# Performance work log

Hardware: AMD Instinct MI355X
Metric: run time of the kernel (lower is better)

Reference implementation:

```python
import jax, jax.numpy as jnp
import numpy as np

N = 20000      # total nodes across the mini-batch of graphs
E = 320000     # edges (avg degree 16)
B = 16         # graphs in the batch
HEADS = 8
EPS_BN = 1e-5
NEG_SLOPE = 0.2


def _lin(k, fan_in, fan_out):
    return (jax.random.normal(k, (fan_in, fan_out), jnp.float32) / np.float32(np.sqrt(fan_in)))


def setup_inputs() -> dict:
    key = jax.random.key(0)
    ks = jax.random.split(key, 24)
    inp = {}
    inp["x"] = jax.random.normal(ks[0], (N, 3), jnp.float32)
    inp["edge_index"] = jax.random.randint(ks[1], (2, E), 0, N, dtype=jnp.int32)
    inp["batch"] = jnp.sort(jax.random.randint(ks[2], (N,), 0, B, dtype=jnp.int32))
    # GATConv params: lin weight [in, heads*out], att_src/att_dst [heads,out], bias [heads*out]
    dims = [(3, 16), (128, 32), (256, 64)]
    for i, (cin, cout) in enumerate(dims, start=1):
        base = 3 + 5 * i
        inp[f"W{i}"] = _lin(ks[base], cin, HEADS * cout)
        inp[f"as{i}"] = jax.random.normal(ks[base + 1], (HEADS, cout), jnp.float32) * 0.1
        inp[f"ad{i}"] = jax.random.normal(ks[base + 2], (HEADS, cout), jnp.float32) * 0.1
        inp[f"b{i}"] = jnp.zeros((HEADS * cout,), jnp.float32)
        inp[f"g{i}"] = jnp.ones((HEADS * cout,), jnp.float32)
        inp[f"be{i}"] = jnp.zeros((HEADS * cout,), jnp.float32)
    inp["fcW"] = _lin(ks[20], 512, 10)
    inp["fcb"] = jnp.zeros((10,), jnp.float32)
    return inp


def gat_layer(x, src, dst, W, a_s, a_d, bias, heads, out_ch):
    n = x.shape[0]
    h = (x @ W).reshape(n, heads, out_ch)              # [N,H,C]
    al_s = jnp.einsum('nhc,hc->nh', h, a_s)            # [N,H]
    al_d = jnp.einsum('nhc,hc->nh', h, a_d)
    e = jax.nn.leaky_relu(al_s[src] + al_d[dst], NEG_SLOPE)   # [E,H]
    m = jax.ops.segment_max(e, dst, num_segments=n)    # per-dst softmax (stable)
    e = jnp.exp(e - m[dst])
    denom = jax.ops.segment_sum(e, dst, num_segments=n)
    alpha = e / (denom[dst] + 1e-16)
    out = jax.ops.segment_sum(h[src] * alpha[:, :, None], dst, num_segments=n)
    return out.reshape(n, heads * out_ch) + bias


def bn_relu(x, g, b):
    mu = x.mean(0)
    var = x.var(0)  # biased, as torch BN uses for normalization
    return jax.nn.relu((x - mu) * jax.lax.rsqrt(var + EPS_BN) * g + b)


def reference(x, edge_index, batch, W1, as1, ad1, b1, g1, be1,
              W2, as2, ad2, b2, g2, be2, W3, as3, ad3, b3, g3, be3, fcW, fcb):
    n = x.shape[0]
    loops = jnp.arange(n, dtype=edge_index.dtype)
    src = jnp.concatenate([edge_index[0], loops])  # add_self_loops=True (PyG default)
    dst = jnp.concatenate([edge_index[1], loops])
    h = bn_relu(gat_layer(x, src, dst, W1, as1, ad1, b1, HEADS, 16), g1, be1)
    h = bn_relu(gat_layer(h, src, dst, W2, as2, ad2, b2, HEADS, 32), g2, be2)
    h = bn_relu(gat_layer(h, src, dst, W3, as3, ad3, b3, HEADS, 64), g3, be3)
    pooled = jax.ops.segment_max(h, batch, num_segments=B)  # global_max_pool
    return pooled @ fcW + fcb
```

## Files before the change

kernel.cpp:

```cpp
#include <hip/hip_runtime.h>
#include <hip/hip_bf16.h>

#define HEADS 8
#define EPS_BN 1e-5f
#define NEG_SLOPE 0.2f
#define BN_NB 256

typedef __attribute__((ext_vector_type(8))) short bf16x8;
typedef __attribute__((ext_vector_type(4))) float f32x4;

__device__ __forceinline__ float bf2f(unsigned short u) {
    return __uint_as_float(((unsigned int)u) << 16);
}

__device__ __forceinline__ unsigned short f2bf(float f) {
    __hip_bfloat16 b = __float2bfloat16(f);
    return *reinterpret_cast<unsigned short*>(&b);
}

__device__ __forceinline__ void gld_lds16(const ushort* g, ushort* l) {
    __builtin_amdgcn_global_load_lds(
        (const __attribute__((address_space(1))) unsigned int*)g,
        (__attribute__((address_space(3))) unsigned int*)l, 16, 0, 0);
}


__global__ void count_kernel(const int* __restrict__ ei, int E, int N, int* __restrict__ counts) {
    int i = blockIdx.x * blockDim.x + threadIdx.x;
    int total = E + N;
    if (i >= total) return;
    int d = (i < E) ? ei[E + i] : (i - E);
    atomicAdd(&counts[d], 1);
}

__global__ __launch_bounds__(1024) void scan_kernel(const int* __restrict__ counts,
                                                    int* __restrict__ offs, int n) {
    __shared__ int tile[1024];
    int tid = threadIdx.x;
    int carry = 0;
    for (int base = 0; base < n; base += 1024) {
        int v = (base + tid < n) ? counts[base + tid] : 0;
        tile[tid] = v;
        __syncthreads();
        for (int off = 1; off < 1024; off <<= 1) {
            int t = (tid >= off) ? tile[tid - off] : 0;
            __syncthreads();
            tile[tid] += t;
            __syncthreads();
        }
        if (base + tid < n) offs[base + tid + 1] = carry + tile[tid];
        carry += tile[1023];
        __syncthreads();
    }
    if (tid == 0) offs[0] = 0;
}

__global__ void scatter_kernel(const int* __restrict__ ei, int E, int N,
                               const int* __restrict__ offs, int* __restrict__ cursor,
                               int* __restrict__ csr_src) {
    int i = blockIdx.x * blockDim.x + threadIdx.x;
    int total = E + N;
    if (i >= total) return;
    int s, d;
    if (i < E) { s = ei[i]; d = ei[E + i]; } else { s = i - E; d = i - E; }
    int slot = atomicAdd(&cursor[d], 1);
    csr_src[offs[d] + slot] = s;
}


__global__ __launch_bounds__(256) void linear1_al_tr_kernel(const float* __restrict__ x,
                                                            const float* __restrict__ W,
                                                            const float* __restrict__ a_s,
                                                            const float* __restrict__ a_d,
                                                            ushort* __restrict__ h,
                                                            float* __restrict__ als,
                                                            float* __restrict__ ald, int N,
                                                            const float* __restrict__ W2,
                                                            ushort* __restrict__ Wt2,
                                                            const float* __restrict__ W3,
                                                            ushort* __restrict__ Wt3) {
    __shared__ float t[32][33];
    int tid = threadIdx.x;
    int bid = blockIdx.x;
    if (bid < 160) {
        const float* Ws; ushort* Wt; int K, Nc, b;
        if (bid < 32) { Ws = W2; Wt = Wt2; K = 128; Nc = 256; b = bid; }
        else          { Ws = W3; Wt = Wt3; K = 256; Nc = 512; b = bid - 32; }
        int nb = Nc / 32;
        int bx = b % nb, by = b / nb;
        int n0 = bx * 32, k0 = by * 32;
        int lx = tid & 31, ly = tid >> 5;
        for (int r = ly; r < 32; r += 8) t[r][lx] = Ws[(size_t)(k0 + r) * Nc + n0 + lx];
        __syncthreads();
        for (int r = ly; r < 32; r += 8) Wt[(size_t)(n0 + r) * K + k0 + lx] = f2bf(t[lx][r]);
    }
    int n = bid * 2 + (tid >> 7);
    int f = tid & 127;
    if (n >= N) return;
    float acc = x[n * 3 + 0] * W[f] + x[n * 3 + 1] * W[128 + f] + x[n * 3 + 2] * W[256 + f];
    h[(size_t)n * 128 + f] = f2bf(acc);
    float s = acc * a_s[f];
    float ds = acc * a_d[f];
    s += __shfl_xor(s, 1);  ds += __shfl_xor(ds, 1);
    s += __shfl_xor(s, 2);  ds += __shfl_xor(ds, 2);
    s += __shfl_xor(s, 4);  ds += __shfl_xor(ds, 4);
    s += __shfl_xor(s, 8);  ds += __shfl_xor(ds, 8);
    if ((f & 15) == 0) {
        int head = f >> 4;
        als[n * 8 + head] = s;
        ald[n * 8 + head] = ds;
    }
}


template<int K, int C>
__global__ __launch_bounds__(256) void mfma_gemm_kernel(const ushort* __restrict__ A,
                                                        const float* __restrict__ scale,
                                                        const float* __restrict__ shift,
                                                        const ushort* __restrict__ Bt,
                                                        ushort* __restrict__ Cout,
                                                        const float* __restrict__ a_s,
                                                        const float* __restrict__ a_d,
                                                        float* __restrict__ als,
                                                        float* __restrict__ ald,
                                                        int M, int Ncols) {
    __shared__ __align__(16) ushort lA[128 * 64];
    __shared__ __align__(16) ushort lB[128 * 64];
    int tid = threadIdx.x;
    int l = tid & 63, w = tid >> 6;
    int m0 = blockIdx.x * 128;
    int n0 = blockIdx.y * 128;
    int wm = w >> 1, wn = w & 1;
    f32x4 zero = {0.f, 0.f, 0.f, 0.f};
    f32x4 acc[4][4];
#pragma unroll
    for (int m = 0; m < 4; ++m)
#pragma unroll
        for (int n = 0; n < 4; ++n) acc[m][n] = zero;

#pragma unroll
    for (int k0 = 0; k0 < K; k0 += 64) {
        if (k0) __syncthreads();
#pragma unroll
        for (int i = 0; i < 4; ++i) {
            int idx = (w * 4 + i) * 64 + l;
            int row = idx >> 3, p = idx & 7;
            int gc = (p ^ (row & 7)) * 8;
            gld_lds16(Bt + (size_t)(n0 + row) * K + k0 + gc, &lB[idx * 8]);
        }
#pragma unroll
        for (int i = 0; i < 4; ++i) {
            int idx = (w * 4 + i) * 64 + l;
            int row = idx >> 3, p = idx & 7;
            int gc = (p ^ (row & 7)) * 8;
            int ar = m0 + row; ar = (ar < M) ? ar : (M - 1);
            int kk = k0 + gc;
            uint4 raw = *(const uint4*)(A + (size_t)ar * K + kk);
            float4 sc0 = *(const float4*)(scale + kk);
            float4 sc1 = *(const float4*)(scale + kk + 4);
            float4 sh0 = *(const float4*)(shift + kk);
            float4 sh1 = *(const float4*)(shift + kk + 4);
            unsigned int rr0 = raw.x, rr1 = raw.y, rr2 = raw.z, rr3 = raw.w;
            float v0, v1;
            unsigned int o0, o1, o2, o3;
            v0 = fmaxf(__uint_as_float(rr0 << 16) * sc0.x + sh0.x, 0.f);
            v1 = fmaxf(__uint_as_float(rr0 & 0xffff0000u) * sc0.y + sh0.y, 0.f);
            o0 = (unsigned int)f2bf(v0) | ((unsigned int)f2bf(v1) << 16);
            v0 = fmaxf(__uint_as_float(rr1 << 16) * sc0.z + sh0.z, 0.f);
            v1 = fmaxf(__uint_as_float(rr1 & 0xffff0000u) * sc0.w + sh0.w, 0.f);
            o1 = (unsigned int)f2bf(v0) | ((unsigned int)f2bf(v1) << 16);
            v0 = fmaxf(__uint_as_float(rr2 << 16) * sc1.x + sh1.x, 0.f);
            v1 = fmaxf(__uint_as_float(rr2 & 0xffff0000u) * sc1.y + sh1.y, 0.f);
            o2 = (unsigned int)f2bf(v0) | ((unsigned int)f2bf(v1) << 16);
            v0 = fmaxf(__uint_as_float(rr3 << 16) * sc1.z + sh1.z, 0.f);
            v1 = fmaxf(__uint_as_float(rr3 & 0xffff0000u) * sc1.w + sh1.w, 0.f);
            o3 = (unsigned int)f2bf(v0) | ((unsigned int)f2bf(v1) << 16);
            uint4 pk = {o0, o1, o2, o3};
            *(uint4*)&lA[idx * 8] = pk;
        }
        __syncthreads();
#pragma unroll
        for (int ks = 0; ks < 2; ++ks) {
            bf16x8 af[4], bfr[4];
#pragma unroll
            for (int m = 0; m < 4; ++m) {
                int row = wm * 64 + m * 16 + (l & 15);
                int cp = (ks * 4 + (l >> 4)) ^ (row & 7);
                af[m] = *(const bf16x8*)&lA[row * 64 + cp * 8];
            }
#pragma unroll
            for (int n = 0; n < 4; ++n) {
                int row = wn * 64 + n * 16 + (l & 15);
                int cp = (ks * 4 + (l >> 4)) ^ (row & 7);
                bfr[n] = *(const bf16x8*)&lB[row * 64 + cp * 8];
            }
#pragma unroll
            for (int m = 0; m < 4; ++m)
#pragma unroll
                for (int n = 0; n < 4; ++n)
                    acc[m][n] = __builtin_amdgcn_mfma_f32_16x16x32_bf16(af[m], bfr[n], acc[m][n], 0, 0, 0);
        }
    }
    int lr = (l >> 4) * 4, lc = l & 15;
#pragma unroll
    for (int m = 0; m < 4; ++m) {
#pragma unroll
        for (int q = 0; q < 4; ++q) {
            int r = m0 + wm * 64 + m * 16 + lr + q;
            if (r < M) {
#pragma unroll
                for (int n = 0; n < 4; ++n) {
                    int c = n0 + wn * 64 + n * 16 + lc;
                    Cout[(size_t)r * Ncols + c] = f2bf(acc[m][n][q]);
                }
            }
        }
    }
    constexpr int GRP = (C == 64) ? 4 : 2;
    constexpr int NGRP = 4 / GRP;
    float asv[4], adv[4];
#pragma unroll
    for (int n = 0; n < 4; ++n) {
        int cc = n0 + wn * 64 + n * 16 + lc;
        asv[n] = a_s[cc];
        adv[n] = a_d[cc];
    }
#pragma unroll
    for (int m = 0; m < 4; ++m) {
#pragma unroll
        for (int q = 0; q < 4; ++q) {
            int r = m0 + wm * 64 + m * 16 + lr + q;
#pragma unroll
            for (int gg = 0; gg < NGRP; ++gg) {
                float s = 0.f, ds = 0.f;
#pragma unroll
                for (int nn = 0; nn < GRP; ++nn) {
                    int n = gg * GRP + nn;
                    s += acc[m][n][q] * asv[n];
                    ds += acc[m][n][q] * adv[n];
                }
                s += __shfl_xor(s, 1);  ds += __shfl_xor(ds, 1);
                s += __shfl_xor(s, 2);  ds += __shfl_xor(ds, 2);
                s += __shfl_xor(s, 4);  ds += __shfl_xor(ds, 4);
                s += __shfl_xor(s, 8);  ds += __shfl_xor(ds, 8);
                if (lc == 0 && r < M) {
                    int head = (n0 + wn * 64 + gg * (GRP * 16)) / C;
                    als[r * 8 + head] = s;
                    ald[r * 8 + head] = ds;
                }
            }
        }
    }
}


template<int CPL>
__device__ __forceinline__ void gather_accum(const ushort* hp, float wt, float* acc) {
    unsigned int u[CPL / 2];
    if constexpr (CPL == 8) {
        uint4 v = *(const uint4*)hp; u[0] = v.x; u[1] = v.y; u[2] = v.z; u[3] = v.w;
    } else if constexpr (CPL == 4) {
        uint2 v = *(const uint2*)hp; u[0] = v.x; u[1] = v.y;
    } else {
        u[0] = *(const unsigned int*)hp;
    }
#pragma unroll
    for (int j = 0; j < CPL / 2; ++j) {
        acc[2 * j]     += wt * __uint_as_float(u[j] << 16);
        acc[2 * j + 1] += wt * __uint_as_float(u[j] & 0xffff0000u);
    }
}

template<int F, int C>
__global__ __launch_bounds__(256) void aggregate_kernel(const ushort* __restrict__ h,
                                                        const float* __restrict__ als,
                                                        const float* __restrict__ ald,
                                                        const int* __restrict__ offs,
                                                        const int* __restrict__ csr_src,
                                                        const float* __restrict__ bias,
                                                        ushort* __restrict__ outbf, int N) {
    constexpr int CPL = F / 64;
    int w = threadIdx.x >> 6, l = threadIdx.x & 63;
    int d = blockIdx.x * 4 + w;
    if (d >= N) return;
    int start = offs[d];
    int deg = offs[d + 1] - start;
    int hf = l >> 3;
    int hw = l & 7;
    int jslot = l >> 3;
    float aldw = ald[d * 8 + hw];

    float acc[CPL];
#pragma unroll
    for (int j = 0; j < CPL; ++j) acc[j] = 0.f;
    float dsum = 0.f;
    float mrun = -1e30f;

    int nfull = deg & ~7;
    for (int eb = 0; eb < nfull; eb += 8) {
        int sE = (l < 8) ? csr_src[start + eb + l] : 0;
        int smy = __shfl(sE, jslot);
        float v = als[smy * 8 + hw] + aldw;
        v = (v > 0.f) ? v : NEG_SLOPE * v;
        float bm = v;
        bm = fmaxf(bm, __shfl_xor(bm, 8));
        bm = fmaxf(bm, __shfl_xor(bm, 16));
        bm = fmaxf(bm, __shfl_xor(bm, 32));
        float mnew = fmaxf(mrun, bm);
        float rs = __expf(mrun - mnew);
        float pw = __expf(v - mnew);
        dsum = dsum * rs + pw;
        float rsg = __shfl(rs, hf);
#pragma unroll
        for (int j = 0; j < CPL; ++j) acc[j] *= rsg;
        mrun = mnew;
#pragma unroll
        for (int j = 0; j < 8; ++j) {
            int sj = __shfl(sE, j);
            float wt = __shfl(pw, (j << 3) + hf);
            gather_accum<CPL>(h + (size_t)sj * F + l * CPL, wt, acc);
        }
    }
    int rem = deg - nfull;
    if (rem) {
        int sE = (l < rem) ? csr_src[start + nfull + l] : 0;
        int smy = __shfl(sE, jslot);
        float v = -1e30f;
        if (jslot < rem) {
            v = als[smy * 8 + hw] + aldw;
            v = (v > 0.f) ? v : NEG_SLOPE * v;
        }
        float bm = v;
        bm = fmaxf(bm, __shfl_xor(bm, 8));
        bm = fmaxf(bm, __shfl_xor(bm, 16));
        bm = fmaxf(bm, __shfl_xor(bm, 32));
        float mnew = fmaxf(mrun, bm);
        float rs = __expf(mrun - mnew);
        float pw = __expf(v - mnew);
        dsum = dsum * rs + pw;
        float rsg = __shfl(rs, hf);
#pragma unroll
        for (int j = 0; j < CPL; ++j) acc[j] *= rsg;
        for (int j = 0; j < rem; ++j) {
            int sj = __shfl(sE, j);
            float wt = __shfl(pw, (j << 3) + hf);
            gather_accum<CPL>(h + (size_t)sj * F + l * CPL, wt, acc);
        }
    }
    dsum += __shfl_xor(dsum, 8);
    dsum += __shfl_xor(dsum, 16);
    dsum += __shfl_xor(dsum, 32);
    float den = __shfl(dsum, hf);
    float inv = 1.0f / (den + 1e-16f);
    int cbase = l * CPL;
#pragma unroll
    for (int j = 0; j < CPL; ++j)
        outbf[(size_t)d * F + cbase + j] = f2bf(acc[j] * inv + bias[cbase + j]);
}


template<int F>
__global__ __launch_bounds__(256) void bnA_kernel(const ushort* __restrict__ xb,
                                                  float* __restrict__ part,
                                                  int N, int npb) {
    constexpr int F4 = F / 4;
    constexpr int RPI = 256 / F4;
    __shared__ float sdata[256 * 8];
    int tid = threadIdx.x;
    int c4 = tid % F4;
    int ro = tid / F4;
    int n0 = blockIdx.x * npb;
    int n1 = n0 + npb;
    if (n1 > N) n1 = N;
    float s0 = 0, s1 = 0, s2 = 0, s3 = 0, q0 = 0, q1 = 0, q2 = 0, q3 = 0;
    for (int r = n0 + ro; r < n1; r += RPI) {
        ushort4 u = *(const ushort4*)(xb + (size_t)r * F + c4 * 4);
        float v0 = bf2f(u.x), v1 = bf2f(u.y), v2 = bf2f(u.z), v3 = bf2f(u.w);
        s0 += v0; s1 += v1; s2 += v2; s3 += v3;
        q0 += v0 * v0; q1 += v1 * v1; q2 += v2 * v2; q3 += v3 * v3;
    }
    float* sp = &sdata[tid * 8];
    sp[0] = s0; sp[1] = s1; sp[2] = s2; sp[3] = s3;
    sp[4] = q0; sp[5] = q1; sp[6] = q2; sp[7] = q3;
    __syncthreads();
    if (tid < F4) {
        float t[8];
#pragma unroll
        for (int k = 0; k < 8; ++k) t[k] = sdata[tid * 8 + k];
        for (int j = 1; j < RPI; ++j) {
            const float* op = &sdata[(j * F4 + tid) * 8];
#pragma unroll
            for (int k = 0; k < 8; ++k) t[k] += op[k];
        }
        float* pb = part + (size_t)blockIdx.x * 2 * F;
#pragma unroll
        for (int k = 0; k < 4; ++k) {
            pb[tid * 4 + k]     = t[k];
            pb[F + tid * 4 + k] = t[4 + k];
        }
    }
}

template<int F>
__global__ void bnB_kernel(const float* __restrict__ part,
                           const float* __restrict__ g, const float* __restrict__ be,
                           float* __restrict__ scale, float* __restrict__ shift, int N) {
    int f = blockIdx.x * blockDim.x + threadIdx.x;
    if (f >= F) return;
    float sum = 0.f, sq = 0.f;
#pragma unroll 4
    for (int j = 0; j < BN_NB; ++j) {
        sum += part[(size_t)j * 2 * F + f];
        sq  += part[(size_t)j * 2 * F + F + f];
    }
    float invN = 1.0f / (float)N;
    float mean = sum * invN;
    float var = sq * invN - mean * mean;
    float sc = g[f] * rsqrtf(var + EPS_BN);
    scale[f] = sc;
    shift[f] = be[f] - mean * sc;
}


__global__ __launch_bounds__(256) void poolA_kernel(const ushort* __restrict__ xb,
                                                    const int* __restrict__ batch,
                                                    const float* __restrict__ scale,
                                                    const float* __restrict__ shift,
                                                    float* __restrict__ pooled8, int N) {
    int tid = threadIdx.x;
    int c4 = tid & 127;
    int ro = tid >> 7;
    int n0 = blockIdx.x * 64;
    int n1 = n0 + 64;
    if (n1 > N) n1 = N;
    float4 sc = ((const float4*)scale)[c4];
    float4 sh = ((const float4*)shift)[c4];
    float* pbase = pooled8 + (size_t)(blockIdx.x & 7) * (16 * 512);
    float m0 = 0.f, m1 = 0.f, m2 = 0.f, m3 = 0.f;
    int cur = -1;
    for (int n = n0 + ro; n < n1; n += 2) {
        int b = batch[n];
        if (b != cur) {
            if (cur >= 0) {
                int base = cur * 512 + c4 * 4;
                atomicMax((int*)&pbase[base],     __float_as_int(m0));
                atomicMax((int*)&pbase[base + 1], __float_as_int(m1));
                atomicMax((int*)&pbase[base + 2], __float_as_int(m2));
                atomicMax((int*)&pbase[base + 3], __float_as_int(m3));
            }
            cur = b;
            m0 = m1 = m2 = m3 = 0.f;
        }
        ushort4 u = *(const ushort4*)(xb + (size_t)n * 512 + c4 * 4);
        m0 = fmaxf(m0, bf2f(u.x) * sc.x + sh.x);
        m1 = fmaxf(m1, bf2f(u.y) * sc.y + sh.y);
        m2 = fmaxf(m2, bf2f(u.z) * sc.z + sh.z);
        m3 = fmaxf(m3, bf2f(u.w) * sc.w + sh.w);
    }
    if (cur >= 0) {
        int base = cur * 512 + c4 * 4;
        atomicMax((int*)&pbase[base],     __float_as_int(m0));
        atomicMax((int*)&pbase[base + 1], __float_as_int(m1));
        atomicMax((int*)&pbase[base + 2], __float_as_int(m2));
        atomicMax((int*)&pbase[base + 3], __float_as_int(m3));
    }
}

__global__ __launch_bounds__(512) void poolFC_kernel(const float* __restrict__ pooled8,
                                                     const float* __restrict__ fcW,
                                                     const float* __restrict__ fcb,
                                                     float* __restrict__ out) {
    __shared__ float sp[16 * 513];
    __shared__ float sw[512 * 10];
    int tid = threadIdx.x;
    for (int c = tid; c < 16 * 512; c += 512) {
        float m = pooled8[c];
#pragma unroll
        for (int k = 1; k < 8; ++k) m = fmaxf(m, pooled8[k * 16 * 512 + c]);
        int b = c >> 9, f = c & 511;
        sp[b * 513 + f] = m;
    }
    for (int i = tid; i < 512 * 10; i += 512) sw[i] = fcW[i];
    __syncthreads();
    if (tid < 160) {
        int b = tid / 10, j = tid % 10;
        float acc = fcb[j];
        const float* spb = &sp[b * 513];
#pragma unroll 8
        for (int f = 0; f < 512; ++f) acc += spb[f] * sw[f * 10 + j];
        out[tid] = acc;
    }
}


extern "C" void kernel_launch(void* const* d_in, const int* in_sizes, int n_in,
                              void* d_out, int out_size, void* d_ws, size_t ws_size,
                              hipStream_t stream) {
    const float* x   = (const float*)d_in[0];
    const int* ei    = (const int*)d_in[1];
    const int* batch = (const int*)d_in[2];
    const float* W1  = (const float*)d_in[3];
    const float* as1 = (const float*)d_in[4];
    const float* ad1 = (const float*)d_in[5];
    const float* b1  = (const float*)d_in[6];
    const float* g1  = (const float*)d_in[7];
    const float* be1 = (const float*)d_in[8];
    const float* W2  = (const float*)d_in[9];
    const float* as2 = (const float*)d_in[10];
    const float* ad2 = (const float*)d_in[11];
    const float* b2  = (const float*)d_in[12];
    const float* g2  = (const float*)d_in[13];
    const float* be2 = (const float*)d_in[14];
    const float* W3  = (const float*)d_in[15];
    const float* as3 = (const float*)d_in[16];
    const float* ad3 = (const float*)d_in[17];
    const float* b3  = (const float*)d_in[18];
    const float* g3  = (const float*)d_in[19];
    const float* be3 = (const float*)d_in[20];
    const float* fcW = (const float*)d_in[21];
    const float* fcb = (const float*)d_in[22];
    float* out = (float*)d_out;

    int N = in_sizes[0] / 3;
    int E = in_sizes[1] / 2;

    char* p = (char*)d_ws;
    auto alloc = [&](size_t bytes) {
        char* r = p;
        p += (bytes + 255) & ~(size_t)255;
        return r;
    };
    char* zbase   = p;
    int*   counts = (int*)alloc((size_t)N * 4);
    int*   cursor = (int*)alloc((size_t)N * 4);
    float* pooled8 = (float*)alloc(8 * 16 * 512 * 4);
    size_t zbytes = (size_t)(p - zbase);
    int*   offs   = (int*)alloc((size_t)(N + 1) * 4);
    int*   csr    = (int*)alloc((size_t)(E + N) * 4);
    ushort* h     = (ushort*)alloc((size_t)N * 512 * 2);
    ushort* aggbf = (ushort*)alloc((size_t)N * 512 * 2);
    ushort* Wt2   = (ushort*)alloc(256 * 128 * 2);
    ushort* Wt3   = (ushort*)alloc(512 * 256 * 2);
    float* als    = (float*)alloc((size_t)N * 8 * 4);
    float* ald    = (float*)alloc((size_t)N * 8 * 4);
    float* bnpart = (float*)alloc((size_t)BN_NB * 1024 * 4);
    float* scale  = (float*)alloc(512 * 4);
    float* shift  = (float*)alloc(512 * 4);

    int total_e = E + N;
    int mtiles = (N + 127) / 128;
    int bnnpb = (N + BN_NB - 1) / BN_NB;
    int ablocks = (N + 3) / 4;
    int pblocks = (N + 63) / 64;

    hipMemsetAsync(zbase, 0, zbytes, stream);

    count_kernel<<<(total_e + 255) / 256, 256, 0, stream>>>(ei, E, N, counts);
    scan_kernel<<<1, 1024, 0, stream>>>(counts, offs, N);
    scatter_kernel<<<(total_e + 255) / 256, 256, 0, stream>>>(ei, E, N, offs, cursor, csr);

    linear1_al_tr_kernel<<<(N + 1) / 2, 256, 0, stream>>>(x, W1, as1, ad1, h, als, ald, N,
                                                          W2, Wt2, W3, Wt3);
    aggregate_kernel<128, 16><<<ablocks, 256, 0, stream>>>(h, als, ald, offs, csr, b1, aggbf, N);
    bnA_kernel<128><<<BN_NB, 256, 0, stream>>>(aggbf, bnpart, N, bnnpb);
    bnB_kernel<128><<<1, 128, 0, stream>>>(bnpart, g1, be1, scale, shift, N);

    mfma_gemm_kernel<128, 32><<<dim3(mtiles, 2), 256, 0, stream>>>(
        aggbf, scale, shift, Wt2, h, as2, ad2, als, ald, N, 256);
    aggregate_kernel<256, 32><<<ablocks, 256, 0, stream>>>(h, als, ald, offs, csr, b2, aggbf, N);
    bnA_kernel<256><<<BN_NB, 256, 0, stream>>>(aggbf, bnpart, N, bnnpb);
    bnB_kernel<256><<<1, 256, 0, stream>>>(bnpart, g2, be2, scale, shift, N);

    mfma_gemm_kernel<256, 64><<<dim3(mtiles, 4), 256, 0, stream>>>(
        aggbf, scale, shift, Wt3, h, as3, ad3, als, ald, N, 512);
    aggregate_kernel<512, 64><<<ablocks, 256, 0, stream>>>(h, als, ald, offs, csr, b3, aggbf, N);
    bnA_kernel<512><<<BN_NB, 256, 0, stream>>>(aggbf, bnpart, N, bnnpb);
    bnB_kernel<512><<<2, 256, 0, stream>>>(bnpart, g3, be3, scale, shift, N);

    poolA_kernel<<<pblocks, 256, 0, stream>>>(aggbf, batch, scale, shift, pooled8, N);
    poolFC_kernel<<<1, 512, 0, stream>>>(pooled8, fcW, fcb, out);
}
```

Baseline: 349.3 us.

## Parallelize CSR offset scan across blocks and stage BN scale/shift in LDS

Replaces the single-block serial-chunk prefix scan over node degree counts with a two-kernel multi-block scan: per-block scans that write block totals, then an add pass where each block sums the preceding totals. This removes the roughly 20 sequential chunk iterations that ran on one CU, at the cost of one extra launch. Separately, the MFMA GEMM now copies the BN scale and shift vectors into shared memory once per block instead of reading them from global memory inside the A-tile load loop. The part buffer holds 64 entries, which limits N to 65536.

```diff
diff --git a/kernel.cpp b/kernel.cpp
--- a/kernel.cpp
+++ b/kernel.cpp
@@ -33,26 +33,37 @@
     atomicAdd(&counts[d], 1);
 }
 
-__global__ __launch_bounds__(1024) void scan_kernel(const int* __restrict__ counts,
-                                                    int* __restrict__ offs, int n) {
+__global__ __launch_bounds__(1024) void scan_block_kernel(const int* __restrict__ counts,
+                                                          int* __restrict__ offs,
+                                                          int* __restrict__ part, int n) {
     __shared__ int tile[1024];
     int tid = threadIdx.x;
-    int carry = 0;
-    for (int base = 0; base < n; base += 1024) {
-        int v = (base + tid < n) ? counts[base + tid] : 0;
-        tile[tid] = v;
+    int gid = blockIdx.x * 1024 + tid;
+    int v = (gid < n) ? counts[gid] : 0;
+    tile[tid] = v;
+    __syncthreads();
+    for (int off = 1; off < 1024; off <<= 1) {
+        int t = (tid >= off) ? tile[tid - off] : 0;
         __syncthreads();
-        for (int off = 1; off < 1024; off <<= 1) {
-            int t = (tid >= off) ? tile[tid - off] : 0;
-            __syncthreads();
-            tile[tid] += t;
-            __syncthreads();
-        }
-        if (base + tid < n) offs[base + tid + 1] = carry + tile[tid];
-        carry += tile[1023];
+        tile[tid] += t;
         __syncthreads();
     }
-    if (tid == 0) offs[0] = 0;
+    if (gid < n) offs[gid + 1] = tile[tid];
+    if (tid == 1023) part[blockIdx.x] = tile[1023];
+}
+
+__global__ __launch_bounds__(1024) void scan_add_kernel(int* __restrict__ offs,
+                                                        const int* __restrict__ part, int n) {
+    __shared__ int base;
+    if (threadIdx.x == 0) {
+        int s = 0;
+        for (int i = 0; i < (int)blockIdx.x; ++i) s += part[i];
+        base = s;
+    }
+    __syncthreads();
+    int gid = blockIdx.x * 1024 + threadIdx.x;
+    if (gid < n) offs[gid + 1] += base;
+    if (gid == 0) offs[0] = 0;
 }
 
 __global__ void scatter_kernel(const int* __restrict__ ei, int E, int N,
@@ -126,17 +137,24 @@
                                                         int M, int Ncols) {
     __shared__ __align__(16) ushort lA[128 * 64];
     __shared__ __align__(16) ushort lB[128 * 64];
+    __shared__ __align__(16) float s_scale[K];
+    __shared__ __align__(16) float s_shift[K];
     int tid = threadIdx.x;
     int l = tid & 63, w = tid >> 6;
     int m0 = blockIdx.x * 128;
     int n0 = blockIdx.y * 128;
     int wm = w >> 1, wn = w & 1;
+    for (int i = tid; i < K; i += 256) {
+        s_scale[i] = scale[i];
+        s_shift[i] = shift[i];
+    }
     f32x4 zero = {0.f, 0.f, 0.f, 0.f};
     f32x4 acc[4][4];
 #pragma unroll
     for (int m = 0; m < 4; ++m)
 #pragma unroll
         for (int n = 0; n < 4; ++n) acc[m][n] = zero;
+    __syncthreads();
 
 #pragma unroll
     for (int k0 = 0; k0 < K; k0 += 64) {
@@ -156,10 +174,10 @@
             int ar = m0 + row; ar = (ar < M) ? ar : (M - 1);
             int kk = k0 + gc;
             uint4 raw = *(const uint4*)(A + (size_t)ar * K + kk);
-            float4 sc0 = *(const float4*)(scale + kk);
-            float4 sc1 = *(const float4*)(scale + kk + 4);
-            float4 sh0 = *(const float4*)(shift + kk);
-            float4 sh1 = *(const float4*)(shift + kk + 4);
+            float4 sc0 = *(const float4*)(s_scale + kk);
+            float4 sc1 = *(const float4*)(s_scale + kk + 4);
+            float4 sh0 = *(const float4*)(s_shift + kk);
+            float4 sh1 = *(const float4*)(s_shift + kk + 4);
             unsigned int rr0 = raw.x, rr1 = raw.y, rr2 = raw.z, rr3 = raw.w;
             float v0, v1;
             unsigned int o0, o1, o2, o3;
@@ -536,6 +554,7 @@
     float* pooled8 = (float*)alloc(8 * 16 * 512 * 4);
     size_t zbytes = (size_t)(p - zbase);
     int*   offs   = (int*)alloc((size_t)(N + 1) * 4);
+    int*   part   = (int*)alloc(64 * 4);
     int*   csr    = (int*)alloc((size_t)(E + N) * 4);
     ushort* h     = (ushort*)alloc((size_t)N * 512 * 2);
     ushort* aggbf = (ushort*)alloc((size_t)N * 512 * 2);
@@ -548,6 +567,7 @@
     float* shift  = (float*)alloc(512 * 4);
 
     int total_e = E + N;
+    int nchunks = (N + 1023) / 1024;
     int mtiles = (N + 127) / 128;
     int bnnpb = (N + BN_NB - 1) / BN_NB;
     int ablocks = (N + 3) / 4;
@@ -556,7 +576,8 @@
     hipMemsetAsync(zbase, 0, zbytes, stream);
 
     count_kernel<<<(total_e + 255) / 256, 256, 0, stream>>>(ei, E, N, counts);
-    scan_kernel<<<1, 1024, 0, stream>>>(counts, offs, N);
+    scan_block_kernel<<<nchunks, 1024, 0, stream>>>(counts, offs, part, N);
+    scan_add_kernel<<<nchunks, 1024, 0, stream>>>(offs, part, N);
     scatter_kernel<<<(total_e + 255) / 256, 256, 0, stream>>>(ei, E, N, offs, cursor, csr);
 
     linear1_al_tr_kernel<<<(N + 1) / 2, 256, 0, stream>>>(x, W1, as1, ad1, h, als, ald, N,
```

After: 318.6 us (median of 2 runs). -8.8%, faster.
